# Performance work log

Hardware: AMD Instinct MI355X
Metric: run time of the kernel (lower is better)

Reference implementation:

```python
import jax, jax.numpy as jnp
import numpy as np

EPS = 1e-5


def conv1x1(x, w, b):
    # x: [b,c,h,w], w: [o,c], b: [o] -> [b,o,h,w]  (1x1 conv == channel matmul)
    return jnp.einsum('bchw,oc->bohw', x, w) + b[None, :, None, None]


def nor_mean_std(x):
    # instance norm over spatial dims (torch calc_mean_std uses unbiased var)
    mean = jnp.mean(x, axis=(2, 3), keepdims=True)
    var = jnp.var(x, axis=(2, 3), keepdims=True, ddof=1)
    return (x - mean) / jnp.sqrt(var + EPS)


def nor_mean(x):
    mean = jnp.mean(x, axis=(2, 3), keepdims=True)
    return x - mean, mean


def net(x, w1, b1, w2, b2):
    return conv1x1(jax.nn.relu(conv1x1(x, w1, b1)), w2, b2)


def setup_inputs() -> dict:
    key = jax.random.key(0)
    ks = jax.random.split(key, 8)
    B, C, H, W = 8, 256, 128, 128
    return {
        'content': jax.random.normal(ks[0], (B, C, H, W), jnp.float32),
        'style': jax.random.normal(ks[1], (B, C, H, W), jnp.float32),
        'w1': jax.random.normal(ks[2], (128, 256), jnp.float32) * 0.05,
        'b1': jax.random.normal(ks[3], (128,), jnp.float32) * 0.05,
        'w2': jax.random.normal(ks[4], (32, 128), jnp.float32) * 0.05,
        'b2': jax.random.normal(ks[5], (32,), jnp.float32) * 0.05,
        'wu': jax.random.normal(ks[6], (256, 32), jnp.float32) * 0.05,
        'bu': jax.random.normal(ks[7], (256,), jnp.float32) * 0.05,
    }


def reference(content, style, w1, b1, w2, b2, wu, bu):
    cF_nor = nor_mean_std(content)
    sF_nor, smean = nor_mean(style)
    cF = net(cF_nor, w1, b1, w2, b2)          # [b,32,h,w]
    sF = net(sF_nor, w1, b1, w2, b2)          # [b,32,h,w]
    b, c, h, w = cF.shape
    hw = h * w
    sf = sF.reshape(b, c, hw)
    # channel covariance: [b,32,32]
    s_cov = jnp.einsum('bcn,bdn->bcd', sf, sf) / hw
    s_cov = jax.nn.softmax(s_cov, axis=-1) * (c ** -0.5)
    gF = jnp.einsum('bcd,bdn->bcn', s_cov, cF.reshape(b, c, hw)).reshape(b, c, h, w)
    gF = conv1x1(gF, wu, bu)                  # [b,256,h,w]
    return gF + smean + content
```

## Files before the change

kernel.cpp:

```cpp
#include <hip/hip_runtime.h>

#define HW 16384
#define C_IN 256
#define C_MID 128
#define C_OUT 32
#define EPSF 1e-5f

typedef __bf16 bf16x8 __attribute__((ext_vector_type(8)));
typedef __bf16 bf16x4 __attribute__((ext_vector_type(4)));
typedef float f32x4 __attribute__((ext_vector_type(4)));

__global__ __launch_bounds__(512) void k_stats7(const float* __restrict__ content,
                                                const float* __restrict__ style,
                                                float* __restrict__ cmean,
                                                float* __restrict__ crstd,
                                                float* __restrict__ smean) {
    const int bc = blockIdx.x;
    const int t = threadIdx.x;
    const f32x4* cp = (const f32x4*)(content + (size_t)bc * HW);
    const f32x4* sp = (const f32x4*)(style + (size_t)bc * HW);
    const int phase = (bc * 257) & 4095;

    f32x4 c0 = cp[(phase + t          ) & 4095];
    f32x4 c1 = cp[(phase + t +  1*512) & 4095];
    f32x4 c2 = cp[(phase + t +  2*512) & 4095];
    f32x4 c3 = cp[(phase + t +  3*512) & 4095];
    f32x4 c4 = cp[(phase + t +  4*512) & 4095];
    f32x4 c5 = cp[(phase + t +  5*512) & 4095];
    f32x4 c6 = cp[(phase + t +  6*512) & 4095];
    f32x4 c7 = cp[(phase + t +  7*512) & 4095];
    f32x4 s0 = __builtin_nontemporal_load(sp + ((phase + t          ) & 4095));
    f32x4 s1 = __builtin_nontemporal_load(sp + ((phase + t +  1*512) & 4095));
    f32x4 s2 = __builtin_nontemporal_load(sp + ((phase + t +  2*512) & 4095));
    f32x4 s3 = __builtin_nontemporal_load(sp + ((phase + t +  3*512) & 4095));
    f32x4 s4 = __builtin_nontemporal_load(sp + ((phase + t +  4*512) & 4095));
    f32x4 s5 = __builtin_nontemporal_load(sp + ((phase + t +  5*512) & 4095));
    f32x4 s6 = __builtin_nontemporal_load(sp + ((phase + t +  6*512) & 4095));
    f32x4 s7 = __builtin_nontemporal_load(sp + ((phase + t +  7*512) & 4095));
    asm volatile("" ::
        "v"(c0), "v"(c1), "v"(c2), "v"(c3), "v"(c4), "v"(c5), "v"(c6), "v"(c7),
        "v"(s0), "v"(s1), "v"(s2), "v"(s3), "v"(s4), "v"(s5), "v"(s6), "v"(s7));

    float cs, cq, ss;
    {
        f32x4 a01 = c0 + c1, a23 = c2 + c3, a45 = c4 + c5, a67 = c6 + c7;
        f32x4 a = (a01 + a23) + (a45 + a67);
        cs = (a[0] + a[1]) + (a[2] + a[3]);
        f32x4 q01 = c0 * c0 + c1 * c1, q23 = c2 * c2 + c3 * c3;
        f32x4 q45 = c4 * c4 + c5 * c5, q67 = c6 * c6 + c7 * c7;
        f32x4 q = (q01 + q23) + (q45 + q67);
        cq = (q[0] + q[1]) + (q[2] + q[3]);
        f32x4 b01 = s0 + s1, b23 = s2 + s3, b45 = s4 + s5, b67 = s6 + s7;
        f32x4 bsum = (b01 + b23) + (b45 + b67);
        ss = (bsum[0] + bsum[1]) + (bsum[2] + bsum[3]);
    }

    #pragma unroll
    for (int d = 32; d > 0; d >>= 1) {
        cs += __shfl_xor(cs, d, 64);
        cq += __shfl_xor(cq, d, 64);
        ss += __shfl_xor(ss, d, 64);
    }
    __shared__ float rs[8], rq[8], rss[8];
    const int wv = t >> 6;
    if ((t & 63) == 0) { rs[wv] = cs; rq[wv] = cq; rss[wv] = ss; }
    __syncthreads();
    if (t == 0) {
        float S = 0.f, Q = 0.f, SS = 0.f;
        #pragma unroll
        for (int i = 0; i < 8; ++i) { S += rs[i]; Q += rq[i]; SS += rss[i]; }
        float n = (float)HW;
        float var = (Q - S * S / n) / (n - 1.f);
        cmean[bc] = S / n;
        crstd[bc] = 1.f / sqrtf(var + EPSF);
        smean[bc] = SS / n;
    }
}

__global__ __launch_bounds__(256) void k_wprep(const float* __restrict__ w1,
                                               const float* __restrict__ b1,
                                               const float* __restrict__ cmean,
                                               const float* __restrict__ crstd,
                                               const float* __restrict__ smean,
                                               __bf16* __restrict__ W1c,
                                               float* __restrict__ bias1c,
                                               __bf16* __restrict__ W1s,
                                               float* __restrict__ bias1s) {
    int o = blockIdx.x, b = blockIdx.y, t = threadIdx.x;
    float w = w1[o * 256 + t];
    float r = crstd[b * 256 + t];
    float wc = w * r;
    W1c[((size_t)(b * 128 + o)) * 256 + t] = (__bf16)wc;
    if (b == 0) W1s[o * 256 + t] = (__bf16)w;
    float pc = wc * cmean[b * 256 + t];
    float ps = w * smean[b * 256 + t];
    __shared__ float rA[256], rB[256];
    rA[t] = pc; rB[t] = ps;
    __syncthreads();
    for (int off = 128; off > 0; off >>= 1) {
        if (t < off) { rA[t] += rA[t + off]; rB[t] += rB[t + off]; }
        __syncthreads();
    }
    if (t == 0) {
        bias1c[b * 128 + o] = b1[o] - rA[0];
        bias1s[b * 128 + o] = b1[o] - rB[0];
    }
}

__global__ __launch_bounds__(256) void k_w2prep(const float* __restrict__ w2,
                                                __bf16* __restrict__ W2b) {
    int i = blockIdx.x * 256 + threadIdx.x;
    if (i < 4096) W2b[i] = (__bf16)w2[i];
}

template <bool NT>
__device__ __forceinline__ float ld_f32(const float* p) {
    if constexpr (NT) return __builtin_nontemporal_load(p);
    else return *p;
}

template <bool NT_X>
__global__ __launch_bounds__(256) void k_net_mfma(const float* __restrict__ x,
                                                  const __bf16* __restrict__ W1,
                                                  const float* __restrict__ bias1,
                                                  const __bf16* __restrict__ W2,
                                                  const float* __restrict__ b2,
                                                  float* __restrict__ outF,
                                                  int w1_per_batch) {
    __shared__ __bf16 Xl[64 * 256];
    __shared__ __bf16 Tl[64 * 128];
    const int tid = threadIdx.x;
    const int l = tid & 63, wv = tid >> 6;
    const int lr = l & 15, g = l >> 4;
    const int sw = (lr & 7) << 4;
    const int p0 = blockIdx.x * 64;
    const int b = blockIdx.y;
    const float* xb = x + (size_t)b * C_IN * HW;

    {
        const int p = wv * 16 + lr;
        const float* xp = xb + p0 + p;
        char* row = (char*)&Xl[p * 256];
        #pragma unroll 4
        for (int cc = 0; cc < 16; ++cc) {
            const int c = cc * 16 + g * 4;
            float f0 = ld_f32<NT_X>(xp + (size_t)(c + 0) * HW);
            float f1 = ld_f32<NT_X>(xp + (size_t)(c + 1) * HW);
            float f2 = ld_f32<NT_X>(xp + (size_t)(c + 2) * HW);
            float f3 = ld_f32<NT_X>(xp + (size_t)(c + 3) * HW);
            bf16x4 v;
            v[0] = (__bf16)f0; v[1] = (__bf16)f1; v[2] = (__bf16)f2; v[3] = (__bf16)f3;
            *(bf16x4*)(row + ((c * 2) ^ sw)) = v;
        }
    }
    __syncthreads();

    const f32x4 zero4 = {0.f, 0.f, 0.f, 0.f};
    f32x4 acc[2][4];
    #pragma unroll
    for (int mt = 0; mt < 2; ++mt)
        #pragma unroll
        for (int nt = 0; nt < 4; ++nt) acc[mt][nt] = zero4;

    const __bf16* W1b = W1 + (w1_per_batch ? ((size_t)b << 15) : 0);
    const __bf16* wrow0 = W1b + (size_t)(wv * 32 + lr) * 256 + g * 8;
    const __bf16* wrow1 = wrow0 + 16 * 256;

    #pragma unroll
    for (int kt = 0; kt < 8; ++kt) {
        bf16x8 a0 = *(const bf16x8*)(wrow0 + kt * 32);
        bf16x8 a1 = *(const bf16x8*)(wrow1 + kt * 32);
        #pragma unroll
        for (int nt = 0; nt < 4; ++nt) {
            const char* xrow = (const char*)&Xl[(nt * 16 + lr) * 256];
            bf16x8 bfr = *(const bf16x8*)(xrow + (((kt * 32 + g * 8) * 2) ^ sw));
            acc[0][nt] = __builtin_amdgcn_mfma_f32_16x16x32_bf16(a0, bfr, acc[0][nt], 0, 0, 0);
            acc[1][nt] = __builtin_amdgcn_mfma_f32_16x16x32_bf16(a1, bfr, acc[1][nt], 0, 0, 0);
        }
    }

    float4 bia[2];
    bia[0] = *(const float4*)&bias1[b * 128 + wv * 32 + g * 4];
    bia[1] = *(const float4*)&bias1[b * 128 + wv * 32 + 16 + g * 4];
    #pragma unroll
    for (int mt = 0; mt < 2; ++mt) {
        #pragma unroll
        for (int nt = 0; nt < 4; ++nt) {
            const int p = nt * 16 + lr;
            char* trow = (char*)&Tl[p * 128];
            const int ob = (wv * 32 + mt * 16 + g * 4) * 2;
            bf16x4 tv;
            tv[0] = (__bf16)fmaxf(acc[mt][nt][0] + bia[mt].x, 0.f);
            tv[1] = (__bf16)fmaxf(acc[mt][nt][1] + bia[mt].y, 0.f);
            tv[2] = (__bf16)fmaxf(acc[mt][nt][2] + bia[mt].z, 0.f);
            tv[3] = (__bf16)fmaxf(acc[mt][nt][3] + bia[mt].w, 0.f);
            *(bf16x4*)(trow + (ob ^ sw)) = tv;
        }
    }
    __syncthreads();

    f32x4 acc2[2];
    acc2[0] = zero4; acc2[1] = zero4;
    const int p = wv * 16 + lr;
    const char* trow = (const char*)&Tl[p * 128];
    const __bf16* w2r0 = W2 + (size_t)lr * 128 + g * 8;
    const __bf16* w2r1 = w2r0 + 16 * 128;
    #pragma unroll
    for (int kt = 0; kt < 4; ++kt) {
        bf16x8 bfr = *(const bf16x8*)(trow + (((kt * 32 + g * 8) * 2) ^ sw));
        bf16x8 a0 = *(const bf16x8*)(w2r0 + kt * 32);
        bf16x8 a1 = *(const bf16x8*)(w2r1 + kt * 32);
        acc2[0] = __builtin_amdgcn_mfma_f32_16x16x32_bf16(a0, bfr, acc2[0], 0, 0, 0);
        acc2[1] = __builtin_amdgcn_mfma_f32_16x16x32_bf16(a1, bfr, acc2[1], 0, 0, 0);
    }
    float4 bb0 = *(const float4*)&b2[g * 4];
    float4 bb1 = *(const float4*)&b2[16 + g * 4];
    float* ob = outF + (size_t)b * C_OUT * HW + p0 + p;
    const int o0 = g * 4;
    ob[(size_t)(o0 + 0) * HW] = acc2[0][0] + bb0.x;
    ob[(size_t)(o0 + 1) * HW] = acc2[0][1] + bb0.y;
    ob[(size_t)(o0 + 2) * HW] = acc2[0][2] + bb0.z;
    ob[(size_t)(o0 + 3) * HW] = acc2[0][3] + bb0.w;
    ob[(size_t)(16 + o0 + 0) * HW] = acc2[1][0] + bb1.x;
    ob[(size_t)(16 + o0 + 1) * HW] = acc2[1][1] + bb1.y;
    ob[(size_t)(16 + o0 + 2) * HW] = acc2[1][2] + bb1.z;
    ob[(size_t)(16 + o0 + 3) * HW] = acc2[1][3] + bb1.w;
}

__global__ __launch_bounds__(256) void k_gram(const float* __restrict__ sF,
                                              float* __restrict__ partial) {
    __shared__ float sS[32 * 257];
    int b = blockIdx.y, sl = blockIdx.x;
    int t = threadIdx.x;
    const float* base = sF + (size_t)b * C_OUT * HW + sl * 1024;
    int i = t >> 3, jb = (t & 7) * 4;
    float acc[4] = {0.f, 0.f, 0.f, 0.f};
    for (int ch = 0; ch < 4; ++ch) {
        __syncthreads();
        #pragma unroll
        for (int r = 0; r < 32; ++r)
            sS[r * 257 + t] = base[(size_t)r * HW + ch * 256 + t];
        __syncthreads();
        for (int n = 0; n < 256; ++n) {
            float si = sS[i * 257 + n];
            #pragma unroll
            for (int q = 0; q < 4; ++q)
                acc[q] = fmaf(si, sS[(jb + q) * 257 + n], acc[q]);
        }
    }
    float* dst = partial + ((size_t)(b * 16 + sl)) * 1024 + t * 4;
    #pragma unroll
    for (int q = 0; q < 4; ++q) dst[q] = acc[q];
}

__global__ __launch_bounds__(1024) void k_softmax(const float* __restrict__ partial,
                                                  float* __restrict__ scov) {
    int b = blockIdx.x;
    int j = threadIdx.x, i = threadIdx.y;
    float v = 0.f;
    #pragma unroll
    for (int s = 0; s < 16; ++s)
        v += partial[((size_t)(b * 16 + s)) * 1024 + i * 32 + j];
    v *= (1.f / (float)HW);
    float m = v;
    #pragma unroll
    for (int d = 16; d > 0; d >>= 1) m = fmaxf(m, __shfl_xor(m, d, 32));
    float e = expf(v - m);
    float sum = e;
    #pragma unroll
    for (int d = 16; d > 0; d >>= 1) sum += __shfl_xor(sum, d, 32);
    scov[(size_t)b * 1024 + i * 32 + j] = e / sum * 0.17677669529663687f;
}

__global__ __launch_bounds__(256) void k_final(const float* __restrict__ cF,
                                               const float* __restrict__ scov,
                                               const float* __restrict__ wu,
                                               const float* __restrict__ bu,
                                               const float* __restrict__ smean,
                                               const float* __restrict__ content,
                                               float* __restrict__ out) {
    __shared__ float sCov[1024];
    __shared__ float sC[32 * 64];
    __shared__ float sG[32 * 64];
    __shared__ float sWu[32 * 260];
    int t = threadIdx.x;
    int p0 = blockIdx.x * 64;
    int b = blockIdx.y;
    #pragma unroll
    for (int q = 0; q < 4; ++q) sCov[t + 256 * q] = scov[(size_t)b * 1024 + t + 256 * q];
    {
        int p = t & 63, rb = t >> 6;
        #pragma unroll
        for (int pass = 0; pass < 8; ++pass) {
            int r = pass * 4 + rb;
            sC[r * 64 + p] = cF[(size_t)b * C_OUT * HW + (size_t)r * HW + p0 + p];
        }
    }
    {
        int k = t & 31, ob = t >> 5;
        #pragma unroll
        for (int pass = 0; pass < 32; ++pass) {
            int o = pass * 8 + ob;
            sWu[k * 260 + o] = wu[o * 32 + k];
        }
    }
    __syncthreads();
    {
        int gp = t & 63, gib = (t >> 6) * 8;
        #pragma unroll
        for (int rr = 0; rr < 8; ++rr) {
            int gi = gib + rr;
            float a = 0.f;
            #pragma unroll
            for (int k = 0; k < 32; ++k)
                a = fmaf(sCov[gi * 32 + k], sC[k * 64 + gp], a);
            sG[gi * 64 + gp] = a;
        }
    }
    __syncthreads();
    int tx = t & 7, ty = t >> 3;
    float acc[8][8];
    #pragma unroll
    for (int i = 0; i < 8; ++i)
        #pragma unroll
        for (int j = 0; j < 8; ++j) acc[i][j] = 0.f;
    #pragma unroll 4
    for (int k = 0; k < 32; ++k) {
        float4 a4a = *(const float4*)&sWu[k * 260 + ty * 8];
        float4 a4b = *(const float4*)&sWu[k * 260 + ty * 8 + 4];
        float4 b4a = *(const float4*)&sG[k * 64 + tx * 8];
        float4 b4b = *(const float4*)&sG[k * 64 + tx * 8 + 4];
        float a[8] = {a4a.x, a4a.y, a4a.z, a4a.w, a4b.x, a4b.y, a4b.z, a4b.w};
        float bb[8] = {b4a.x, b4a.y, b4a.z, b4a.w, b4b.x, b4b.y, b4b.z, b4b.w};
        #pragma unroll
        for (int i = 0; i < 8; ++i)
            #pragma unroll
            for (int j = 0; j < 8; ++j)
                acc[i][j] = fmaf(a[i], bb[j], acc[i][j]);
    }
    #pragma unroll
    for (int i = 0; i < 8; ++i) {
        int o = ty * 8 + i;
        float add = bu[o] + smean[b * 256 + o];
        const float* csrc = content + (size_t)b * C_IN * HW + (size_t)o * HW + p0 + tx * 8;
        float* dst = out + (size_t)b * C_IN * HW + (size_t)o * HW + p0 + tx * 8;
        float4 c0 = *(const float4*)csrc;
        float4 c1 = *(const float4*)(csrc + 4);
        f32x4 r0 = {acc[i][0] + add + c0.x, acc[i][1] + add + c0.y,
                    acc[i][2] + add + c0.z, acc[i][3] + add + c0.w};
        f32x4 r1 = {acc[i][4] + add + c1.x, acc[i][5] + add + c1.y,
                    acc[i][6] + add + c1.z, acc[i][7] + add + c1.w};
        __builtin_nontemporal_store(r0, (f32x4*)dst);
        __builtin_nontemporal_store(r1, (f32x4*)(dst + 4));
    }
}

extern "C" void kernel_launch(void* const* d_in, const int* in_sizes, int n_in,
                              void* d_out, int out_size, void* d_ws, size_t ws_size,
                              hipStream_t stream) {
    const float* content = (const float*)d_in[0];
    const float* style   = (const float*)d_in[1];
    const float* w1      = (const float*)d_in[2];
    const float* b1      = (const float*)d_in[3];
    const float* w2      = (const float*)d_in[4];
    const float* b2      = (const float*)d_in[5];
    const float* wu      = (const float*)d_in[6];
    const float* bu      = (const float*)d_in[7];
    float* out = (float*)d_out;
    float* ws  = (float*)d_ws;

    float* cmean   = ws;
    float* crstd   = ws + 2048;
    float* smean   = ws + 4096;
    float* scov    = ws + 6144;
    __bf16* W2b    = (__bf16*)(ws + 6144);
    float* bias1c  = ws + 8192;
    float* bias1s  = ws + 9216;
    float* partial = ws + 14336;
    __bf16* W1c    = (__bf16*)(ws + 14336);
    __bf16* W1s    = (__bf16*)(ws + 145408);
    float* cF      = ws + 161792;
    float* sF      = cF + 4194304;

    k_stats7<<<dim3(2048), 512, 0, stream>>>(content, style, cmean, crstd, smean);
    k_wprep<<<dim3(128, 8), 256, 0, stream>>>(w1, b1, cmean, crstd, smean,
                                              W1c, bias1c, W1s, bias1s);
    k_w2prep<<<dim3(16), 256, 0, stream>>>(w2, W2b);
    k_net_mfma<false><<<dim3(256, 8), 256, 0, stream>>>(content, W1c, bias1c, W2b, b2, cF, 1);
    k_net_mfma<true><<<dim3(256, 8), 256, 0, stream>>>(style, W1s, bias1s, W2b, b2, sF, 0);
    k_gram<<<dim3(16, 8), 256, 0, stream>>>(sF, partial);
    k_softmax<<<dim3(8), dim3(32, 32), 0, stream>>>(partial, scov);
    k_final<<<dim3(256, 8), 256, 0, stream>>>(cF, scov, wu, bu, smean, content, out);
}
```

Baseline: 246.5 us.

## Stage bf16 copies of content and style in stats pass for later kernels

The stats kernel now also writes bf16 copies of content and style when the workspace is large enough. A new MLP kernel reads those bf16 tensors instead of fp32, and the final kernel reads the residual content in bf16 too. The goal is to halve the bytes read by the two network passes and by the final residual read. In exchange the stats pass gains an extra write of both inputs, and the residual add loses precision, which may hurt accuracy. The old fp32 path remains as a fallback when the workspace is too small.

```diff
diff --git a/kernel.cpp b/kernel.cpp
--- a/kernel.cpp
+++ b/kernel.cpp
@@ -10,47 +10,62 @@
 typedef __bf16 bf16x4 __attribute__((ext_vector_type(4)));
 typedef float f32x4 __attribute__((ext_vector_type(4)));
 
-__global__ __launch_bounds__(512) void k_stats7(const float* __restrict__ content,
+__device__ __forceinline__ bf16x4 cvt4(f32x4 v) {
+    bf16x4 r;
+    r[0] = (__bf16)v[0]; r[1] = (__bf16)v[1];
+    r[2] = (__bf16)v[2]; r[3] = (__bf16)v[3];
+    return r;
+}
+
+template <int MODE>
+__global__ __launch_bounds__(512) void k_stats8(const float* __restrict__ content,
                                                 const float* __restrict__ style,
                                                 float* __restrict__ cmean,
                                                 float* __restrict__ crstd,
-                                                float* __restrict__ smean) {
+                                                float* __restrict__ smean,
+                                                __bf16* __restrict__ cbf,
+                                                __bf16* __restrict__ sbf) {
     const int bc = blockIdx.x;
     const int t = threadIdx.x;
     const f32x4* cp = (const f32x4*)(content + (size_t)bc * HW);
     const f32x4* sp = (const f32x4*)(style + (size_t)bc * HW);
     const int phase = (bc * 257) & 4095;
 
-    f32x4 c0 = cp[(phase + t          ) & 4095];
-    f32x4 c1 = cp[(phase + t +  1*512) & 4095];
-    f32x4 c2 = cp[(phase + t +  2*512) & 4095];
-    f32x4 c3 = cp[(phase + t +  3*512) & 4095];
-    f32x4 c4 = cp[(phase + t +  4*512) & 4095];
-    f32x4 c5 = cp[(phase + t +  5*512) & 4095];
-    f32x4 c6 = cp[(phase + t +  6*512) & 4095];
-    f32x4 c7 = cp[(phase + t +  7*512) & 4095];
-    f32x4 s0 = __builtin_nontemporal_load(sp + ((phase + t          ) & 4095));
-    f32x4 s1 = __builtin_nontemporal_load(sp + ((phase + t +  1*512) & 4095));
-    f32x4 s2 = __builtin_nontemporal_load(sp + ((phase + t +  2*512) & 4095));
-    f32x4 s3 = __builtin_nontemporal_load(sp + ((phase + t +  3*512) & 4095));
-    f32x4 s4 = __builtin_nontemporal_load(sp + ((phase + t +  4*512) & 4095));
-    f32x4 s5 = __builtin_nontemporal_load(sp + ((phase + t +  5*512) & 4095));
-    f32x4 s6 = __builtin_nontemporal_load(sp + ((phase + t +  6*512) & 4095));
-    f32x4 s7 = __builtin_nontemporal_load(sp + ((phase + t +  7*512) & 4095));
+    int idx[8];
+    #pragma unroll
+    for (int i = 0; i < 8; ++i) idx[i] = (phase + t + i * 512) & 4095;
+
+    f32x4 c[8], s[8];
+    #pragma unroll
+    for (int i = 0; i < 8; ++i)
+        c[i] = (MODE == 1) ? __builtin_nontemporal_load(cp + idx[i]) : cp[idx[i]];
+    #pragma unroll
+    for (int i = 0; i < 8; ++i)
+        s[i] = __builtin_nontemporal_load(sp + idx[i]);
     asm volatile("" ::
-        "v"(c0), "v"(c1), "v"(c2), "v"(c3), "v"(c4), "v"(c5), "v"(c6), "v"(c7),
-        "v"(s0), "v"(s1), "v"(s2), "v"(s3), "v"(s4), "v"(s5), "v"(s6), "v"(s7));
+        "v"(c[0]), "v"(c[1]), "v"(c[2]), "v"(c[3]), "v"(c[4]), "v"(c[5]), "v"(c[6]), "v"(c[7]),
+        "v"(s[0]), "v"(s[1]), "v"(s[2]), "v"(s[3]), "v"(s[4]), "v"(s[5]), "v"(s[6]), "v"(s[7]));
+
+    if constexpr (MODE == 1) {
+        bf16x4* cb = (bf16x4*)(cbf + (size_t)bc * HW);
+        bf16x4* sb = (bf16x4*)(sbf + (size_t)bc * HW);
+        #pragma unroll
+        for (int i = 0; i < 8; ++i) {
+            cb[idx[i]] = cvt4(c[i]);
+            sb[idx[i]] = cvt4(s[i]);
+        }
+    }
 
     float cs, cq, ss;
     {
-        f32x4 a01 = c0 + c1, a23 = c2 + c3, a45 = c4 + c5, a67 = c6 + c7;
+        f32x4 a01 = c[0] + c[1], a23 = c[2] + c[3], a45 = c[4] + c[5], a67 = c[6] + c[7];
         f32x4 a = (a01 + a23) + (a45 + a67);
         cs = (a[0] + a[1]) + (a[2] + a[3]);
-        f32x4 q01 = c0 * c0 + c1 * c1, q23 = c2 * c2 + c3 * c3;
-        f32x4 q45 = c4 * c4 + c5 * c5, q67 = c6 * c6 + c7 * c7;
+        f32x4 q01 = c[0]*c[0] + c[1]*c[1], q23 = c[2]*c[2] + c[3]*c[3];
+        f32x4 q45 = c[4]*c[4] + c[5]*c[5], q67 = c[6]*c[6] + c[7]*c[7];
         f32x4 q = (q01 + q23) + (q45 + q67);
         cq = (q[0] + q[1]) + (q[2] + q[3]);
-        f32x4 b01 = s0 + s1, b23 = s2 + s3, b45 = s4 + s5, b67 = s6 + s7;
+        f32x4 b01 = s[0] + s[1], b23 = s[2] + s[3], b45 = s[4] + s[5], b67 = s[6] + s[7];
         f32x4 bsum = (b01 + b23) + (b45 + b67);
         ss = (bsum[0] + bsum[1]) + (bsum[2] + bsum[3]);
     }
@@ -227,6 +242,112 @@
     ob[(size_t)(16 + o0 + 3) * HW] = acc2[1][3] + bb1.w;
 }
 
+__global__ __launch_bounds__(256) void k_net_mfma_bf(const __bf16* __restrict__ x,
+                                                     const __bf16* __restrict__ W1,
+                                                     const float* __restrict__ bias1,
+                                                     const __bf16* __restrict__ W2,
+                                                     const float* __restrict__ b2,
+                                                     float* __restrict__ outF,
+                                                     int w1_per_batch) {
+    __shared__ __bf16 Xl[64 * 256];
+    __shared__ __bf16 Tl[64 * 128];
+    const int tid = threadIdx.x;
+    const int l = tid & 63, wv = tid >> 6;
+    const int lr = l & 15, g = l >> 4;
+    const int sw = (lr & 7) << 4;
+    const int p0 = blockIdx.x * 64;
+    const int b = blockIdx.y;
+    const __bf16* xb = x + (size_t)b * C_IN * HW;
+
+    {
+        const int p = wv * 16 + lr;
+        const __bf16* xp = xb + p0 + p;
+        char* row = (char*)&Xl[p * 256];
+        #pragma unroll 4
+        for (int cc = 0; cc < 16; ++cc) {
+            const int c = cc * 16 + g * 4;
+            bf16x4 v;
+            v[0] = xp[(size_t)(c + 0) * HW];
+            v[1] = xp[(size_t)(c + 1) * HW];
+            v[2] = xp[(size_t)(c + 2) * HW];
+            v[3] = xp[(size_t)(c + 3) * HW];
+            *(bf16x4*)(row + ((c * 2) ^ sw)) = v;
+        }
+    }
+    __syncthreads();
+
+    const f32x4 zero4 = {0.f, 0.f, 0.f, 0.f};
+    f32x4 acc[2][4];
+    #pragma unroll
+    for (int mt = 0; mt < 2; ++mt)
+        #pragma unroll
+        for (int nt = 0; nt < 4; ++nt) acc[mt][nt] = zero4;
+
+    const __bf16* W1b = W1 + (w1_per_batch ? ((size_t)b << 15) : 0);
+    const __bf16* wrow0 = W1b + (size_t)(wv * 32 + lr) * 256 + g * 8;
+    const __bf16* wrow1 = wrow0 + 16 * 256;
+
+    #pragma unroll
+    for (int kt = 0; kt < 8; ++kt) {
+        bf16x8 a0 = *(const bf16x8*)(wrow0 + kt * 32);
+        bf16x8 a1 = *(const bf16x8*)(wrow1 + kt * 32);
+        #pragma unroll
+        for (int nt = 0; nt < 4; ++nt) {
+            const char* xrow = (const char*)&Xl[(nt * 16 + lr) * 256];
+            bf16x8 bfr = *(const bf16x8*)(xrow + (((kt * 32 + g * 8) * 2) ^ sw));
+            acc[0][nt] = __builtin_amdgcn_mfma_f32_16x16x32_bf16(a0, bfr, acc[0][nt], 0, 0, 0);
+            acc[1][nt] = __builtin_amdgcn_mfma_f32_16x16x32_bf16(a1, bfr, acc[1][nt], 0, 0, 0);
+        }
+    }
+
+    float4 bia[2];
+    bia[0] = *(const float4*)&bias1[b * 128 + wv * 32 + g * 4];
+    bia[1] = *(const float4*)&bias1[b * 128 + wv * 32 + 16 + g * 4];
+    #pragma unroll
+    for (int mt = 0; mt < 2; ++mt) {
+        #pragma unroll
+        for (int nt = 0; nt < 4; ++nt) {
+            const int p = nt * 16 + lr;
+            char* trow = (char*)&Tl[p * 128];
+            const int ob = (wv * 32 + mt * 16 + g * 4) * 2;
+            bf16x4 tv;
+            tv[0] = (__bf16)fmaxf(acc[mt][nt][0] + bia[mt].x, 0.f);
+            tv[1] = (__bf16)fmaxf(acc[mt][nt][1] + bia[mt].y, 0.f);
+            tv[2] = (__bf16)fmaxf(acc[mt][nt][2] + bia[mt].z, 0.f);
+            tv[3] = (__bf16)fmaxf(acc[mt][nt][3] + bia[mt].w, 0.f);
+            *(bf16x4*)(trow + (ob ^ sw)) = tv;
+        }
+    }
+    __syncthreads();
+
+    f32x4 acc2[2];
+    acc2[0] = zero4; acc2[1] = zero4;
+    const int p = wv * 16 + lr;
+    const char* trow = (const char*)&Tl[p * 128];
+    const __bf16* w2r0 = W2 + (size_t)lr * 128 + g * 8;
+    const __bf16* w2r1 = w2r0 + 16 * 128;
+    #pragma unroll
+    for (int kt = 0; kt < 4; ++kt) {
+        bf16x8 bfr = *(const bf16x8*)(trow + (((kt * 32 + g * 8) * 2) ^ sw));
+        bf16x8 a0 = *(const bf16x8*)(w2r0 + kt * 32);
+        bf16x8 a1 = *(const bf16x8*)(w2r1 + kt * 32);
+        acc2[0] = __builtin_amdgcn_mfma_f32_16x16x32_bf16(a0, bfr, acc2[0], 0, 0, 0);
+        acc2[1] = __builtin_amdgcn_mfma_f32_16x16x32_bf16(a1, bfr, acc2[1], 0, 0, 0);
+    }
+    float4 bb0 = *(const float4*)&b2[g * 4];
+    float4 bb1 = *(const float4*)&b2[16 + g * 4];
+    float* ob = outF + (size_t)b * C_OUT * HW + p0 + p;
+    const int o0 = g * 4;
+    ob[(size_t)(o0 + 0) * HW] = acc2[0][0] + bb0.x;
+    ob[(size_t)(o0 + 1) * HW] = acc2[0][1] + bb0.y;
+    ob[(size_t)(o0 + 2) * HW] = acc2[0][2] + bb0.z;
+    ob[(size_t)(o0 + 3) * HW] = acc2[0][3] + bb0.w;
+    ob[(size_t)(16 + o0 + 0) * HW] = acc2[1][0] + bb1.x;
+    ob[(size_t)(16 + o0 + 1) * HW] = acc2[1][1] + bb1.y;
+    ob[(size_t)(16 + o0 + 2) * HW] = acc2[1][2] + bb1.z;
+    ob[(size_t)(16 + o0 + 3) * HW] = acc2[1][3] + bb1.w;
+}
+
 __global__ __launch_bounds__(256) void k_gram(const float* __restrict__ sF,
                                               float* __restrict__ partial) {
     __shared__ float sS[32 * 257];
@@ -272,12 +393,14 @@
     scov[(size_t)b * 1024 + i * 32 + j] = e / sum * 0.17677669529663687f;
 }
 
+template <bool CONTENT_BF16>
 __global__ __launch_bounds__(256) void k_final(const float* __restrict__ cF,
                                                const float* __restrict__ scov,
                                                const float* __restrict__ wu,
                                                const float* __restrict__ bu,
                                                const float* __restrict__ smean,
                                                const float* __restrict__ content,
+                                               const __bf16* __restrict__ cbf,
                                                float* __restrict__ out) {
     __shared__ float sCov[1024];
     __shared__ float sC[32 * 64];
@@ -342,14 +465,24 @@
     for (int i = 0; i < 8; ++i) {
         int o = ty * 8 + i;
         float add = bu[o] + smean[b * 256 + o];
-        const float* csrc = content + (size_t)b * C_IN * HW + (size_t)o * HW + p0 + tx * 8;
         float* dst = out + (size_t)b * C_IN * HW + (size_t)o * HW + p0 + tx * 8;
-        float4 c0 = *(const float4*)csrc;
-        float4 c1 = *(const float4*)(csrc + 4);
-        f32x4 r0 = {acc[i][0] + add + c0.x, acc[i][1] + add + c0.y,
-                    acc[i][2] + add + c0.z, acc[i][3] + add + c0.w};
-        f32x4 r1 = {acc[i][4] + add + c1.x, acc[i][5] + add + c1.y,
-                    acc[i][6] + add + c1.z, acc[i][7] + add + c1.w};
+        float cv[8];
+        if constexpr (CONTENT_BF16) {
+            const __bf16* csrc = cbf + (size_t)b * C_IN * HW + (size_t)o * HW + p0 + tx * 8;
+            bf16x8 cvv = *(const bf16x8*)csrc;
+            #pragma unroll
+            for (int q = 0; q < 8; ++q) cv[q] = (float)cvv[q];
+        } else {
+            const float* csrc = content + (size_t)b * C_IN * HW + (size_t)o * HW + p0 + tx * 8;
+            float4 c0 = *(const float4*)csrc;
+            float4 c1 = *(const float4*)(csrc + 4);
+            cv[0] = c0.x; cv[1] = c0.y; cv[2] = c0.z; cv[3] = c0.w;
+            cv[4] = c1.x; cv[5] = c1.y; cv[6] = c1.z; cv[7] = c1.w;
+        }
+        f32x4 r0 = {acc[i][0] + add + cv[0], acc[i][1] + add + cv[1],
+                    acc[i][2] + add + cv[2], acc[i][3] + add + cv[3]};
+        f32x4 r1 = {acc[i][4] + add + cv[4], acc[i][5] + add + cv[5],
+                    acc[i][6] + add + cv[6], acc[i][7] + add + cv[7]};
         __builtin_nontemporal_store(r0, (f32x4*)dst);
         __builtin_nontemporal_store(r1, (f32x4*)(dst + 4));
     }
@@ -369,26 +502,57 @@
     float* out = (float*)d_out;
     float* ws  = (float*)d_ws;
 
-    float* cmean   = ws;
-    float* crstd   = ws + 2048;
-    float* smean   = ws + 4096;
-    float* scov    = ws + 6144;
-    __bf16* W2b    = (__bf16*)(ws + 6144);
-    float* bias1c  = ws + 8192;
-    float* bias1s  = ws + 9216;
-    float* partial = ws + 14336;
-    __bf16* W1c    = (__bf16*)(ws + 14336);
-    __bf16* W1s    = (__bf16*)(ws + 145408);
-    float* cF      = ws + 161792;
-    float* sF      = cF + 4194304;
-
-    k_stats7<<<dim3(2048), 512, 0, stream>>>(content, style, cmean, crstd, smean);
-    k_wprep<<<dim3(128, 8), 256, 0, stream>>>(w1, b1, cmean, crstd, smean,
-                                              W1c, bias1c, W1s, bias1s);
-    k_w2prep<<<dim3(16), 256, 0, stream>>>(w2, W2b);
-    k_net_mfma<false><<<dim3(256, 8), 256, 0, stream>>>(content, W1c, bias1c, W2b, b2, cF, 1);
-    k_net_mfma<true><<<dim3(256, 8), 256, 0, stream>>>(style, W1s, bias1s, W2b, b2, sF, 0);
-    k_gram<<<dim3(16, 8), 256, 0, stream>>>(sF, partial);
-    k_softmax<<<dim3(8), dim3(32, 32), 0, stream>>>(partial, scov);
-    k_final<<<dim3(256, 8), 256, 0, stream>>>(cF, scov, wu, bu, smean, content, out);
-}
+    const size_t NEED = 42240000ull * sizeof(float);
+    if (ws_size >= NEED) {
+        float* cmean   = ws;
+        float* crstd   = ws + 2048;
+        float* smean   = ws + 4096;
+        float* scov    = ws + 6144;
+        float* bias1c  = ws + 14336;
+        float* bias1s  = ws + 15360;
+        __bf16* W2b    = (__bf16*)(ws + 16384);
+        __bf16* W1s    = (__bf16*)(ws + 18432);
+        __bf16* W1c    = (__bf16*)(ws + 34816);
+        float* partial = ws + 165888;
+        float* cF      = ws + 296960;
+        float* sF      = cF + 4194304;
+        __bf16* cbf    = (__bf16*)(ws + 8685568);
+        __bf16* sbf    = (__bf16*)(ws + 8685568 + 16777216);
+
+        k_stats8<1><<<dim3(2048), 512, 0, stream>>>(content, style, cmean, crstd, smean, cbf, sbf);
+        k_wprep<<<dim3(128, 8), 256, 0, stream>>>(w1, b1, cmean, crstd, smean,
+                                                  W1c, bias1c, W1s, bias1s);
+        k_w2prep<<<dim3(16), 256, 0, stream>>>(w2, W2b);
+        k_net_mfma_bf<<<dim3(256, 8), 256, 0, stream>>>(cbf, W1c, bias1c, W2b, b2, cF, 1);
+        k_net_mfma_bf<<<dim3(256, 8), 256, 0, stream>>>(sbf, W1s, bias1s, W2b, b2, sF, 0);
+        k_gram<<<dim3(16, 8), 256, 0, stream>>>(sF, partial);
+        k_softmax<<<dim3(8), dim3(32, 32), 0, stream>>>(partial, scov);
+        k_final<true><<<dim3(256, 8), 256, 0, stream>>>(cF, scov, wu, bu, smean,
+                                                        content, cbf, out);
+    } else {
+        float* cmean   = ws;
+        float* crstd   = ws + 2048;
+        float* smean   = ws + 4096;
+        float* scov    = ws + 6144;
+        __bf16* W2b    = (__bf16*)(ws + 6144);
+        float* bias1c  = ws + 8192;
+        float* bias1s  = ws + 9216;
+        float* partial = ws + 14336;
+        __bf16* W1c    = (__bf16*)(ws + 14336);
+        __bf16* W1s    = (__bf16*)(ws + 145408);
+        float* cF      = ws + 161792;
+        float* sF      = cF + 4194304;
+
+        k_stats8<0><<<dim3(2048), 512, 0, stream>>>(content, style, cmean, crstd, smean,
+                                                    nullptr, nullptr);
+        k_wprep<<<dim3(128, 8), 256, 0, stream>>>(w1, b1, cmean, crstd, smean,
+                                                  W1c, bias1c, W1s, bias1s);
+        k_w2prep<<<dim3(16), 256, 0, stream>>>(w2, W2b);
+        k_net_mfma<false><<<dim3(256, 8), 256, 0, stream>>>(content, W1c, bias1c, W2b, b2, cF, 1);
+        k_net_mfma<true><<<dim3(256, 8), 256, 0, stream>>>(style, W1s, bias1s, W2b, b2, sF, 0);
+        k_gram<<<dim3(16, 8), 256, 0, stream>>>(sF, partial);
+        k_softmax<<<dim3(8), dim3(32, 32), 0, stream>>>(partial, scov);
+        k_final<false><<<dim3(256, 8), 256, 0, stream>>>(cF, scov, wu, bu, smean,
+                                                         content, nullptr, out);
+    }
+}
```

Result: no change. 246.3 us (-0.1%).
